# Optimization experiments

Hardware: AMD Instinct MI355X
Metric: run time of the kernel (lower is better)

Reference implementation:

```python
import jax, jax.numpy as jnp
import numpy as np

V = 6890          # SMPL vertex count
RAYS, POINTS = 256, 64
LATENT_DIM = 16
RES_HI, RES_LO = 10, 4


def posenc(x, res):
    # NeRF-style encoding: [x, sin(2^k x), cos(2^k x)] for k in 0..res-1 -> D*(1+2*res)
    freqs = 2.0 ** jnp.arange(res, dtype=x.dtype)            # [res]
    xf = x[..., None, :] * freqs[:, None]                    # [..., res, D]
    n = x.shape[:-1]
    s = jnp.sin(xf).reshape(*n, -1)
    c = jnp.cos(xf).reshape(*n, -1)
    return jnp.concatenate([x, s, c], axis=-1)


def setup_inputs() -> dict:
    key = jax.random.key(0)
    ks = jax.random.split(key, 12)
    inp = {}
    inp['pts'] = jax.random.normal(ks[0], (RAYS, POINTS, 6), jnp.float32)
    inp['keypoints'] = jax.random.normal(ks[1], (V, 3), jnp.float32)
    # invertible per-vertex 4x4 transforms: identity + small noise, stored [4,4,V]
    noise = 0.1 * jax.random.normal(ks[2], (4, 4, V), jnp.float32)
    inp['trans_kp'] = jnp.eye(4, dtype=jnp.float32)[:, :, None] + noise
    inp['neighbors'] = jax.random.randint(ks[3], (V, 7), 0, V, jnp.int32)
    inp['rest_pose'] = jax.random.normal(ks[4], (V, 3), jnp.float32)
    inp['latent'] = jax.random.normal(ks[5], (V, LATENT_DIM), jnp.float32)
    d_in = 7 * ((2 * RES_HI + 1) * 4 + LATENT_DIM)  # 700
    inp['W1'] = 0.05 * jax.random.normal(ks[6], (d_in, 256), jnp.float32)
    inp['b1'] = jnp.zeros((256,), jnp.float32)
    inp['W2'] = 0.05 * jax.random.normal(ks[7], (256, 256), jnp.float32)
    inp['b2'] = jnp.zeros((256,), jnp.float32)
    inp['W3'] = 0.05 * jax.random.normal(ks[8], (256, 256), jnp.float32)
    inp['b3'] = jnp.zeros((256,), jnp.float32)
    return inp


def reference(pts, keypoints, trans_kp, neighbors, rest_pose, latent,
              W1, b1, W2, b2, W3, b3):
    rays, points, _ = pts.shape
    p, view_dir = jnp.split(pts, 2, axis=-1)
    p = p.reshape(rays * points, 3)                          # [N,3]

    # brute-force 1-NN of p into keypoints
    d2 = ((p * p).sum(-1, keepdims=True)
          - 2.0 * p @ keypoints.T
          + (keypoints * keypoints).sum(-1))                 # [N,V]
    knn_index = jnp.argmin(d2, axis=1)                       # [N]

    # inverse transforms, keep rotation part: [3,3,V]
    T = jnp.linalg.inv(jnp.transpose(trans_kp, (2, 0, 1)))   # [V,4,4]
    R = jnp.transpose(T, (1, 2, 0))[:3, :3]                  # [3,3,V]

    vidx = neighbors[knn_index]                              # [N,7]
    vdist = p[:, None, :] - keypoints[vidx]                  # [N,7,3]

    diff = p - keypoints[knn_index]                          # [N,3]
    Rg = R[:, :, knn_index]                                  # [3,3,N]
    direction = jnp.einsum('ijn,nj->ni', Rg, diff)           # [N,3]
    nrm = jnp.linalg.norm(direction, axis=-1, keepdims=True)
    direction = direction / jnp.maximum(nrm, 1e-12)

    vfeat = jnp.concatenate(
        [rest_pose[vidx].reshape(-1, 21),
         jnp.linalg.norm(vdist, axis=-1)], axis=-1)          # [N,28]
    lfeat = latent[vidx].reshape(-1, 7 * latent.shape[1])    # [N,112]

    h = jnp.concatenate([posenc(vfeat, RES_HI), lfeat], -1)  # [N,700]
    h = jax.nn.relu(h @ W1 + b1)
    h = jax.nn.relu(h @ W2 + b2)
    h = h @ W3 + b3                                          # [N,256]

    out = jnp.concatenate([h, posenc(direction, RES_LO)], -1)  # [N,283]
    return out.reshape(rays, points, -1)
```

## Files before the change

kernel.cpp:

```cpp
#include <hip/hip_runtime.h>
#include <hip/hip_bf16.h>
#include <math.h>

#define V_N   6890
#define N_PTS 16384
#define D_IN  700
#define D_INP 704
#define D_HID 256
#define D_OUT 283
#define NCHUNK 32
#define CHUNK  216
#define GAP_EPS 1e-4f

#define RINV4_OFF 0
#define KP4_OFF   82688
#define RP4_OFF   110272
#define PB4_OFF   170640
#define WT1_OFF   2267792
#define WT2_OFF   2357904
#define WT3_OFF   2390672
#define X_OFF     2423440

typedef __attribute__((ext_vector_type(8))) short short8;
typedef __attribute__((ext_vector_type(4))) float f32x4;

__device__ __forceinline__ unsigned short f2bf(float f) {
    unsigned int u = __builtin_bit_cast(unsigned int, f);
    u += 0x7fffu + ((u >> 16) & 1u);
    return (unsigned short)(u >> 16);
}

__device__ __forceinline__ float fsin(float x) {
    return __builtin_amdgcn_sinf(__builtin_amdgcn_fractf(x * 0.15915494309189535f));
}
__device__ __forceinline__ float fcos(float x) {
    return __builtin_amdgcn_cosf(__builtin_amdgcn_fractf(x * 0.15915494309189535f));
}

__device__ __forceinline__ void glds16(const void* g, void* l) {
    __builtin_amdgcn_global_load_lds(
        (const __attribute__((address_space(1))) void*)g,
        (__attribute__((address_space(3))) void*)l, 16, 0, 0);
}

__device__ __forceinline__ int swzoff(int r, int sub) {
    return ((r << 2) | (sub ^ ((r >> 1) & 3))) << 4;
}

__device__ __forceinline__ int rescan64(const float* __restrict__ pts,
                                        const float4* __restrict__ kp4,
                                        int nn, int lane) {
    double pxd = (double)pts[nn*6+0], pyd = (double)pts[nn*6+1], pzd = (double)pts[nn*6+2];
    double ppd = pxd*pxd + pyd*pyd + pzd*pzd;
    double best = 1e300; int bbi = 0x7fffffff;
    for (int jj = lane; jj < V_N; jj += 64) {
        float4 k = kp4[jj];
        double kx = (double)k.x, ky = (double)k.y, kz = (double)k.z;
        double d = ppd - 2.0*(pxd*kx + pyd*ky + pzd*kz) + (kx*kx + ky*ky + kz*kz);
        if (d < best || (d == best && jj < bbi)) { best = d; bbi = jj; }
    }
#pragma unroll
    for (int off = 32; off >= 1; off >>= 1) {
        double od = __shfl_xor(best, off);
        int    oi = __shfl_xor(bbi, off);
        if (od < best || (od == best && oi < bbi)) { best = od; bbi = oi; }
    }
    return bbi;
}

#define SCAN_BLOCKS 2048
#define PREP_BLOCKS 27
__global__ __launch_bounds__(256) void prep_scan_kernel(
    const float* __restrict__ pts, const float* __restrict__ keyp,
    const float* __restrict__ trans, const float* __restrict__ restp,
    const float* __restrict__ W1, const float* __restrict__ W2,
    const float* __restrict__ W3,
    float4* __restrict__ rinv4, float4* __restrict__ kp4, float4* __restrict__ rp4,
    unsigned short* __restrict__ wt1, unsigned short* __restrict__ wt2,
    unsigned short* __restrict__ wt3, float4* __restrict__ pb4)
{
    __shared__ float4 s_kp[CHUNK];
    int bx = blockIdx.x, tid = threadIdx.x;

    if (bx < SCAN_BLOCKS) {
        int c = bx >> 6;
        int n = (bx & 63) * 256 + tid;
        int v0 = c * CHUNK;
        int nv = min(V_N - v0, CHUNK);
        if (tid < nv) {
            int v = v0 + tid;
            float kx = keyp[v*3+0], ky = keyp[v*3+1], kz = keyp[v*3+2];
            s_kp[tid] = make_float4(kx, ky, kz, kx*kx + ky*ky + kz*kz);
        }
        __syncthreads();

        float px2n = -2.0f * pts[n*6+0], py2n = -2.0f * pts[n*6+1], pz2n = -2.0f * pts[n*6+2];
        float m1 = 1e30f, m2 = 1e30f;
        int bi = 0x7fffffff;

#define KNN_STEP(kk, jj)                                                    \
    {                                                                       \
        float d = __builtin_fmaf(px2n, kk.x,                                \
                  __builtin_fmaf(py2n, kk.y,                                \
                  __builtin_fmaf(pz2n, kk.z, kk.w)));                       \
        bool lt = d < m1;                                                   \
        bi = lt ? (jj) : bi;                                                \
        m2 = __builtin_amdgcn_fmed3f(m1, m2, d);                            \
        m1 = fminf(m1, d);                                                  \
    }
        int j = 0;
        for (; j + 4 <= nv; j += 4) {
            float4 k0 = s_kp[j], k1 = s_kp[j+1], k2 = s_kp[j+2], k3 = s_kp[j+3];
            KNN_STEP(k0, v0+j); KNN_STEP(k1, v0+j+1);
            KNN_STEP(k2, v0+j+2); KNN_STEP(k3, v0+j+3);
        }
        for (; j < nv; ++j) {
            float4 k0 = s_kp[j];
            KNN_STEP(k0, v0+j);
        }
#undef KNN_STEP
        pb4[(size_t)n * NCHUNK + c] = make_float4(m1, m2, __int_as_float(bi), 0.0f);

    } else if (bx < SCAN_BLOCKS + PREP_BLOCKS) {
        int v = (bx - SCAN_BLOCKS) * 256 + tid;
        if (v >= V_N) return;
        float m[16];
#pragma unroll
        for (int i = 0; i < 16; ++i) m[i] = trans[i * V_N + v];

        float i0  =  m[5]*m[10]*m[15] - m[5]*m[11]*m[14] - m[9]*m[6]*m[15] + m[9]*m[7]*m[14] + m[13]*m[6]*m[11] - m[13]*m[7]*m[10];
        float i4  = -m[4]*m[10]*m[15] + m[4]*m[11]*m[14] + m[8]*m[6]*m[15] - m[8]*m[7]*m[14] - m[12]*m[6]*m[11] + m[12]*m[7]*m[10];
        float i8  =  m[4]*m[9]*m[15]  - m[4]*m[11]*m[13] - m[8]*m[5]*m[15] + m[8]*m[7]*m[13] + m[12]*m[5]*m[11] - m[12]*m[7]*m[9];
        float i12 = -m[4]*m[9]*m[14]  + m[4]*m[10]*m[13] + m[8]*m[5]*m[14] - m[8]*m[6]*m[13] - m[12]*m[5]*m[10] + m[12]*m[6]*m[9];
        float i1  = -m[1]*m[10]*m[15] + m[1]*m[11]*m[14] + m[9]*m[2]*m[15] - m[9]*m[3]*m[14] - m[13]*m[2]*m[11] + m[13]*m[3]*m[10];
        float i5  =  m[0]*m[10]*m[15] - m[0]*m[11]*m[14] - m[8]*m[2]*m[15] + m[8]*m[3]*m[14] + m[12]*m[2]*m[11] - m[12]*m[3]*m[10];
        float i9  = -m[0]*m[9]*m[15]  + m[0]*m[11]*m[13] + m[8]*m[1]*m[15] - m[8]*m[3]*m[13] - m[12]*m[1]*m[11] + m[12]*m[3]*m[9];
        float i2  =  m[1]*m[6]*m[15]  - m[1]*m[7]*m[14]  - m[5]*m[2]*m[15] + m[5]*m[3]*m[14] + m[13]*m[2]*m[7]  - m[13]*m[3]*m[6];
        float i6  = -m[0]*m[6]*m[15]  + m[0]*m[7]*m[14]  + m[4]*m[2]*m[15] - m[4]*m[3]*m[14] - m[12]*m[2]*m[7]  + m[12]*m[3]*m[6];
        float i10 =  m[0]*m[5]*m[15]  - m[0]*m[7]*m[13]  - m[4]*m[1]*m[15] + m[4]*m[3]*m[13] + m[12]*m[1]*m[7]  - m[12]*m[3]*m[5];

        float det = m[0]*i0 + m[1]*i4 + m[2]*i8 + m[3]*i12;
        float id = 1.0f / det;
        rinv4[v*3+0] = make_float4(i0*id, i1*id, i2*id, i4*id);
        rinv4[v*3+1] = make_float4(i5*id, i6*id, i8*id, i9*id);
        rinv4[v*3+2] = make_float4(i10*id, 0.0f, 0.0f, 0.0f);

        float kx = keyp[v*3], ky = keyp[v*3+1], kz = keyp[v*3+2];
        kp4[v] = make_float4(kx, ky, kz, kx*kx + ky*ky + kz*kz);
        rp4[v] = make_float4(restp[v*3], restp[v*3+1], restp[v*3+2], 0.0f);
    } else {
        int idx = (bx - SCAN_BLOCKS - PREP_BLOCKS) * 256 + tid;
        const int N1 = 256 * D_INP;
        const int N2 = 256 * 256;
        if (idx < N1) {
            int n = idx / D_INP, k = idx - n * D_INP;
            float v = (k < D_IN) ? W1[k * 256 + n] : 0.0f;
            wt1[n * D_INP + k] = f2bf(v);
        } else if (idx < N1 + N2) {
            int t = idx - N1;
            int n = t >> 8, k = t & 255;
            wt2[n * 256 + k] = f2bf(W2[k * 256 + n]);
        } else if (idx < N1 + 2 * N2) {
            int t = idx - N1 - N2;
            int n = t >> 8, k = t & 255;
            wt3[n * 256 + k] = f2bf(W3[k * 256 + n]);
        }
    }
}

__global__ __launch_bounds__(256) void feat_kernel(
    const float* __restrict__ pts, const int* __restrict__ neigh,
    const float* __restrict__ latent, const float4* __restrict__ rinv4,
    const float4* __restrict__ kp4, const float4* __restrict__ rp4,
    const float4* __restrict__ pb4, unsigned short* __restrict__ X,
    float* __restrict__ out)
{
    __shared__ float s_vf[4][2][29];
    __shared__ float s_dir[4][2][4];

    int t = threadIdx.x;
    int w = t >> 6, lane = t & 63;
    int n0 = blockIdx.x * 8 + w * 2;
    int ph = lane >> 5, g = lane & 31;

    float pxA = pts[n0*6+0],     pyA = pts[n0*6+1],     pzA = pts[n0*6+2];
    float pxB = pts[(n0+1)*6+0], pyB = pts[(n0+1)*6+1], pzB = pts[(n0+1)*6+2];

    float4 P = pb4[(size_t)(n0 + ph) * NCHUNK + g];
    float m1 = P.x, m2 = P.y;
    int   bi = __float_as_int(P.z);
#pragma unroll
    for (int off = 1; off <= 16; off <<= 1) {
        float o1 = __shfl_xor(m1, off);
        float o2 = __shfl_xor(m2, off);
        int   ob = __shfl_xor(bi, off);
        float nm2 = fminf(fminf(m2, o2), fmaxf(m1, o1));
        bool take = (o1 < m1) || (o1 == m1 && ob < bi);
        bi = take ? ob : bi;
        m1 = fminf(m1, o1);
        m2 = nm2;
    }
    unsigned long long ambmask = __ballot(m2 - m1 < GAP_EPS);
    if (ambmask & 1ull) {
        int r = rescan64(pts, kp4, n0, lane);
        if (ph == 0) bi = r;
    }
    if (ambmask & (1ull << 32)) {
        int r = rescan64(pts, kp4, n0 + 1, lane);
        if (ph == 1) bi = r;
    }

    int p = ph, j = g;
    int k8 = bi;
    float px = p ? pxB : pxA, py = p ? pyB : pyA, pz = p ? pzB : pzA;

    int v7 = 0;
    if (j < 7) {
        v7 = neigh[k8*7 + j];
        float4 kq = kp4[v7];
        float4 rq = rp4[v7];
        float dx = px - kq.x, dy = py - kq.y, dz = pz - kq.z;
        s_vf[w][p][j*3+0] = rq.x;
        s_vf[w][p][j*3+1] = rq.y;
        s_vf[w][p][j*3+2] = rq.z;
        s_vf[w][p][21+j]  = sqrtf(dx*dx + dy*dy + dz*dz);
    } else if (j == 7) {
        float4 kq = kp4[k8];
        float ddx = px - kq.x, ddy = py - kq.y, ddz = pz - kq.z;
        float4 R0 = rinv4[k8*3+0];
        float4 R1 = rinv4[k8*3+1];
        float4 R2 = rinv4[k8*3+2];
        float d0 = R0.x*ddx + R0.y*ddy + R0.z*ddz;
        float d1 = R0.w*ddx + R1.x*ddy + R1.y*ddz;
        float d2 = R1.z*ddx + R1.w*ddy + R2.x*ddz;
        float nrm = fmaxf(sqrtf(d0*d0 + d1*d1 + d2*d2), 1e-12f);
        s_dir[w][p][0] = d0/nrm; s_dir[w][p][1] = d1/nrm; s_dir[w][p][2] = d2/nrm;
    }

#pragma unroll
    for (int pp = 0; pp < 2; ++pp) {
        int n = n0 + pp;
        float dir0 = s_dir[w][pp][0];
        float dir1 = s_dir[w][pp][1];
        float dir2 = s_dir[w][pp][2];

        if (lane < 27) {
            float val;
            if (lane < 3) {
                val = (lane == 0) ? dir0 : (lane == 1) ? dir1 : dir2;
            } else {
                int tt = (lane < 15) ? lane - 3 : lane - 15;
                int m = tt % 3;
                float db = (m == 0) ? dir0 : (m == 1) ? dir1 : dir2;
                float a = db * (float)(1 << (tt/3));
                val = (lane < 15) ? fsin(a) : fcos(a);
            }
            out[(size_t)n*D_OUT + 256 + lane] = val;
        }

#pragma unroll
        for (int it = 0; it < 3; ++it) {
            int base = it * 256 + (lane << 2);
            bool in_range = base < D_INP;
            int region = (base < 28) ? 0 : (base < 308) ? 1 : (base < 588) ? 2
                       : (base < 700) ? 3 : 4;

            int t0 = (region == 1) ? base - 28 : (region == 2) ? base - 308 : 0;
            int q = t0 / 28;
            int r = t0 - q * 28;
            float f0 = (float)(1 << q);
            float a[4];
#pragma unroll
            for (int jj = 0; jj < 4; ++jj) {
                int rj; float fj;
                if (region == 0) { rj = base + jj; fj = 1.0f; }
                else if (region <= 2) {
                    rj = r + jj; fj = f0;
                    if (rj >= 28) { rj -= 28; fj = f0 * 2.0f; }
                } else { rj = 0; fj = 0.0f; }
                a[jj] = s_vf[w][pp][rj] * fj;
            }
            int idxc = (region == 3) ? (base - 588) >> 4 : 0;
            int vL = __shfl(v7, pp*32 + idxc);

            unsigned short r0, r1, r2, r3;
            if (region == 0) {
                r0 = f2bf(a[0]); r1 = f2bf(a[1]); r2 = f2bf(a[2]); r3 = f2bf(a[3]);
            } else if (region == 1) {
                r0 = f2bf(fsin(a[0])); r1 = f2bf(fsin(a[1]));
                r2 = f2bf(fsin(a[2])); r3 = f2bf(fsin(a[3]));
            } else if (region == 2) {
                r0 = f2bf(fcos(a[0])); r1 = f2bf(fcos(a[1]));
                r2 = f2bf(fcos(a[2])); r3 = f2bf(fcos(a[3]));
            } else if (region == 3) {
                int t3 = base - 588;
                float4 lv = *(const float4*)&latent[vL * 16 + (t3 & 15)];
                r0 = f2bf(lv.x); r1 = f2bf(lv.y); r2 = f2bf(lv.z); r3 = f2bf(lv.w);
            } else {
                r0 = r1 = r2 = r3 = 0;
            }
            if (in_range)
                *(ushort4*)&X[(size_t)n * D_INP + base] = make_ushort4(r0, r1, r2, r3);
        }
    }
}

#define HLD 264
__global__ __launch_bounds__(512) void mlp_kernel(
    const unsigned short* __restrict__ X,
    const unsigned short* __restrict__ wt1,
    const unsigned short* __restrict__ wt2,
    const unsigned short* __restrict__ wt3,
    const float* __restrict__ b1, const float* __restrict__ b2,
    const float* __restrict__ b3, float* __restrict__ out)
{
    __shared__ unsigned short As[64 * 32];
    __shared__ unsigned short Ws[256 * 32];
    __shared__ unsigned short H1[64 * HLD];
    __shared__ unsigned short H2[64 * HLD];

    int t = threadIdx.x, l = t & 63, w = t >> 6;
    int bm = blockIdx.x * 64;
    int mbase = (w >> 2) * 32, nbase = (w & 3) * 64;
    int lrow = l & 15, lk = (l >> 4) * 8, sub = l >> 4;
    int col0 = l & 15, rquad = (l >> 4) * 4;

    f32x4 acc[2][4];
    short8 af[2], bf[4];

#pragma unroll
    for (int mi = 0; mi < 2; ++mi)
#pragma unroll
        for (int ni = 0; ni < 4; ++ni) acc[mi][ni] = {0.f, 0.f, 0.f, 0.f};

    for (int k0 = 0; k0 < D_INP; k0 += 32) {
        if (t < 256) {
            int r = t >> 2;
            int sg = (t & 3) ^ ((r >> 1) & 3);
            glds16(X + (size_t)(bm + r) * D_INP + k0 + sg * 8, (char*)As + t * 16);
        }
#pragma unroll
        for (int i = 0; i < 2; ++i) {
            int c = i * 512 + t;
            int r = c >> 2;
            int sg = (c & 3) ^ ((r >> 1) & 3);
            glds16(wt1 + (size_t)r * D_INP + k0 + sg * 8, (char*)Ws + (size_t)c * 16);
        }
        __syncthreads();
#pragma unroll
        for (int mi = 0; mi < 2; ++mi)
            af[mi] = *(const short8*)((const char*)As + swzoff(mbase + mi*16 + lrow, sub));
#pragma unroll
        for (int ni = 0; ni < 4; ++ni)
            bf[ni] = *(const short8*)((const char*)Ws + swzoff(nbase + ni*16 + lrow, sub));
#pragma unroll
        for (int mi = 0; mi < 2; ++mi)
#pragma unroll
            for (int ni = 0; ni < 4; ++ni)
                acc[mi][ni] = __builtin_amdgcn_mfma_f32_16x16x32_bf16(
                    af[mi], bf[ni], acc[mi][ni], 0, 0, 0);
        __syncthreads();
    }
#pragma unroll
    for (int mi = 0; mi < 2; ++mi)
#pragma unroll
        for (int ni = 0; ni < 4; ++ni) {
            int col = nbase + ni * 16 + col0;
            float bv = b1[col];
#pragma unroll
            for (int r = 0; r < 4; ++r) {
                int row = mbase + mi * 16 + rquad + r;
                H1[row * HLD + col] = f2bf(fmaxf(acc[mi][ni][r] + bv, 0.0f));
            }
        }
    __syncthreads();

#pragma unroll
    for (int mi = 0; mi < 2; ++mi)
#pragma unroll
        for (int ni = 0; ni < 4; ++ni) acc[mi][ni] = {0.f, 0.f, 0.f, 0.f};

    for (int k0 = 0; k0 < D_HID; k0 += 32) {
#pragma unroll
        for (int i = 0; i < 2; ++i) {
            int c = i * 512 + t;
            int r = c >> 2;
            int sg = (c & 3) ^ ((r >> 1) & 3);
            glds16(wt2 + (size_t)r * D_HID + k0 + sg * 8, (char*)Ws + (size_t)c * 16);
        }
        __syncthreads();
#pragma unroll
        for (int mi = 0; mi < 2; ++mi)
            af[mi] = *(const short8*)&H1[(mbase + mi * 16 + lrow) * HLD + k0 + lk];
#pragma unroll
        for (int ni = 0; ni < 4; ++ni)
            bf[ni] = *(const short8*)((const char*)Ws + swzoff(nbase + ni*16 + lrow, sub));
#pragma unroll
        for (int mi = 0; mi < 2; ++mi)
#pragma unroll
            for (int ni = 0; ni < 4; ++ni)
                acc[mi][ni] = __builtin_amdgcn_mfma_f32_16x16x32_bf16(
                    af[mi], bf[ni], acc[mi][ni], 0, 0, 0);
        __syncthreads();
    }
#pragma unroll
    for (int mi = 0; mi < 2; ++mi)
#pragma unroll
        for (int ni = 0; ni < 4; ++ni) {
            int col = nbase + ni * 16 + col0;
            float bv = b2[col];
#pragma unroll
            for (int r = 0; r < 4; ++r) {
                int row = mbase + mi * 16 + rquad + r;
                H2[row * HLD + col] = f2bf(fmaxf(acc[mi][ni][r] + bv, 0.0f));
            }
        }
    __syncthreads();

#pragma unroll
    for (int mi = 0; mi < 2; ++mi)
#pragma unroll
        for (int ni = 0; ni < 4; ++ni) acc[mi][ni] = {0.f, 0.f, 0.f, 0.f};

    for (int k0 = 0; k0 < D_HID; k0 += 32) {
#pragma unroll
        for (int i = 0; i < 2; ++i) {
            int c = i * 512 + t;
            int r = c >> 2;
            int sg = (c & 3) ^ ((r >> 1) & 3);
            glds16(wt3 + (size_t)r * D_HID + k0 + sg * 8, (char*)Ws + (size_t)c * 16);
        }
        __syncthreads();
#pragma unroll
        for (int mi = 0; mi < 2; ++mi)
            af[mi] = *(const short8*)&H2[(mbase + mi * 16 + lrow) * HLD + k0 + lk];
#pragma unroll
        for (int ni = 0; ni < 4; ++ni)
            bf[ni] = *(const short8*)((const char*)Ws + swzoff(nbase + ni*16 + lrow, sub));
#pragma unroll
        for (int mi = 0; mi < 2; ++mi)
#pragma unroll
            for (int ni = 0; ni < 4; ++ni)
                acc[mi][ni] = __builtin_amdgcn_mfma_f32_16x16x32_bf16(
                    af[mi], bf[ni], acc[mi][ni], 0, 0, 0);
        __syncthreads();
    }
#pragma unroll
    for (int mi = 0; mi < 2; ++mi)
#pragma unroll
        for (int ni = 0; ni < 4; ++ni) {
            int col = nbase + ni * 16 + col0;
            float bv = b3[col];
#pragma unroll
            for (int r = 0; r < 4; ++r) {
                int row = bm + mbase + mi * 16 + rquad + r;
                out[(size_t)row * D_OUT + col] = acc[mi][ni][r] + bv;
            }
        }
}

extern "C" void kernel_launch(void* const* d_in, const int* in_sizes, int n_in,
                              void* d_out, int out_size, void* d_ws, size_t ws_size,
                              hipStream_t stream) {
    const float* pts    = (const float*)d_in[0];
    const float* keyp   = (const float*)d_in[1];
    const float* trans  = (const float*)d_in[2];
    const int*   neigh  = (const int*)d_in[3];
    const float* restp  = (const float*)d_in[4];
    const float* latent = (const float*)d_in[5];
    const float* W1     = (const float*)d_in[6];
    const float* b1     = (const float*)d_in[7];
    const float* W2     = (const float*)d_in[8];
    const float* b2     = (const float*)d_in[9];
    const float* W3     = (const float*)d_in[10];
    const float* b3     = (const float*)d_in[11];
    float* out = (float*)d_out;

    float* wsf = (float*)d_ws;
    float4*         rinv4 = (float4*)(wsf + RINV4_OFF);
    float4*         kp4   = (float4*)(wsf + KP4_OFF);
    float4*         rp4   = (float4*)(wsf + RP4_OFF);
    float4*         pb4   = (float4*)(wsf + PB4_OFF);
    unsigned short* wt1   = (unsigned short*)(wsf + WT1_OFF);
    unsigned short* wt2   = (unsigned short*)(wsf + WT2_OFF);
    unsigned short* wt3   = (unsigned short*)(wsf + WT3_OFF);
    unsigned short* X     = (unsigned short*)(wsf + X_OFF);

    int wconv_blocks = (256*D_INP + 2*256*256 + 255) / 256;
    prep_scan_kernel<<<SCAN_BLOCKS + PREP_BLOCKS + wconv_blocks, 256, 0, stream>>>(
        pts, keyp, trans, restp, W1, W2, W3, rinv4, kp4, rp4, wt1, wt2, wt3, pb4);
    feat_kernel<<<N_PTS/8, 256, 0, stream>>>(pts, neigh, latent, rinv4,
                                             kp4, rp4, pb4, X, out);
    mlp_kernel<<<N_PTS/64, 512, 0, stream>>>(X, wt1, wt2, wt3, b1, b2, b3, out);
}
```

Before: 173.7 us.

## Double-buffer MLP shared-memory tiles and widen KNN unroll to eight

The MLP kernel now keeps two shared-memory buffers for the activation and weight tiles and issues the next K-slice's global-to-LDS loads before computing on the current one. It also prefetches the first weight tile of layers 2 and 3 during the previous layer's epilogue. The point is to hide global load latency behind the MFMA work and to drop one barrier per K step. Separately, the KNN scan inner loop is unrolled by 8 instead of 4. This raises LDS use, which may lower occupancy, and raises register pressure in the scan.

```diff
diff --git a/kernel.cpp b/kernel.cpp
--- a/kernel.cpp
+++ b/kernel.cpp
@@ -109,10 +109,13 @@
         m1 = fminf(m1, d);                                                  \
     }
         int j = 0;
-        for (; j + 4 <= nv; j += 4) {
-            float4 k0 = s_kp[j], k1 = s_kp[j+1], k2 = s_kp[j+2], k3 = s_kp[j+3];
-            KNN_STEP(k0, v0+j); KNN_STEP(k1, v0+j+1);
+        for (; j + 8 <= nv; j += 8) {
+            float4 k0 = s_kp[j],   k1 = s_kp[j+1], k2 = s_kp[j+2], k3 = s_kp[j+3];
+            float4 k4 = s_kp[j+4], k5 = s_kp[j+5], k6 = s_kp[j+6], k7 = s_kp[j+7];
+            KNN_STEP(k0, v0+j);   KNN_STEP(k1, v0+j+1);
             KNN_STEP(k2, v0+j+2); KNN_STEP(k3, v0+j+3);
+            KNN_STEP(k4, v0+j+4); KNN_STEP(k5, v0+j+5);
+            KNN_STEP(k6, v0+j+6); KNN_STEP(k7, v0+j+7);
         }
         for (; j < nv; ++j) {
             float4 k0 = s_kp[j];
@@ -314,8 +317,8 @@
     const float* __restrict__ b1, const float* __restrict__ b2,
     const float* __restrict__ b3, float* __restrict__ out)
 {
-    __shared__ unsigned short As[64 * 32];
-    __shared__ unsigned short Ws[256 * 32];
+    __shared__ unsigned short As[2][64 * 32];
+    __shared__ unsigned short Ws[2][256 * 32];
     __shared__ unsigned short H1[64 * HLD];
     __shared__ unsigned short H2[64 * HLD];
 
@@ -328,31 +331,44 @@
     f32x4 acc[2][4];
     short8 af[2], bf[4];
 
-#pragma unroll
-    for (int mi = 0; mi < 2; ++mi)
-#pragma unroll
-        for (int ni = 0; ni < 4; ++ni) acc[mi][ni] = {0.f, 0.f, 0.f, 0.f};
-
-    for (int k0 = 0; k0 < D_INP; k0 += 32) {
+    auto stageA = [&](int buf, int k0) {
         if (t < 256) {
-            int r = t >> 2;
-            int sg = (t & 3) ^ ((r >> 1) & 3);
-            glds16(X + (size_t)(bm + r) * D_INP + k0 + sg * 8, (char*)As + t * 16);
-        }
+            int r = t >> 2, sg = (t & 3) ^ ((r >> 1) & 3);
+            glds16(X + (size_t)(bm + r) * D_INP + k0 + sg * 8,
+                   (char*)As[buf] + t * 16);
+        }
+    };
+    auto stageW = [&](int buf, const unsigned short* wsrc, int ld, int k0) {
 #pragma unroll
         for (int i = 0; i < 2; ++i) {
             int c = i * 512 + t;
-            int r = c >> 2;
-            int sg = (c & 3) ^ ((r >> 1) & 3);
-            glds16(wt1 + (size_t)r * D_INP + k0 + sg * 8, (char*)Ws + (size_t)c * 16);
-        }
-        __syncthreads();
+            int r = c >> 2, sg = (c & 3) ^ ((r >> 1) & 3);
+            glds16(wsrc + (size_t)r * ld + k0 + sg * 8,
+                   (char*)Ws[buf] + (size_t)c * 16);
+        }
+    };
+
+#pragma unroll
+    for (int mi = 0; mi < 2; ++mi)
+#pragma unroll
+        for (int ni = 0; ni < 4; ++ni) acc[mi][ni] = {0.f, 0.f, 0.f, 0.f};
+
+    stageA(0, 0);
+    stageW(0, wt1, D_INP, 0);
+    __syncthreads();
+    const int NK1 = D_INP / 32;
+    for (int ks = 0; ks < NK1; ++ks) {
+        int cur = ks & 1;
+        if (ks + 1 < NK1) {
+            stageA(cur ^ 1, (ks + 1) * 32);
+            stageW(cur ^ 1, wt1, D_INP, (ks + 1) * 32);
+        }
 #pragma unroll
         for (int mi = 0; mi < 2; ++mi)
-            af[mi] = *(const short8*)((const char*)As + swzoff(mbase + mi*16 + lrow, sub));
+            af[mi] = *(const short8*)((const char*)As[cur] + swzoff(mbase + mi*16 + lrow, sub));
 #pragma unroll
         for (int ni = 0; ni < 4; ++ni)
-            bf[ni] = *(const short8*)((const char*)Ws + swzoff(nbase + ni*16 + lrow, sub));
+            bf[ni] = *(const short8*)((const char*)Ws[cur] + swzoff(nbase + ni*16 + lrow, sub));
 #pragma unroll
         for (int mi = 0; mi < 2; ++mi)
 #pragma unroll
@@ -361,6 +377,7 @@
                     af[mi], bf[ni], acc[mi][ni], 0, 0, 0);
         __syncthreads();
     }
+    stageW(0, wt2, D_HID, 0);
 #pragma unroll
     for (int mi = 0; mi < 2; ++mi)
 #pragma unroll
@@ -380,21 +397,16 @@
 #pragma unroll
         for (int ni = 0; ni < 4; ++ni) acc[mi][ni] = {0.f, 0.f, 0.f, 0.f};
 
-    for (int k0 = 0; k0 < D_HID; k0 += 32) {
-#pragma unroll
-        for (int i = 0; i < 2; ++i) {
-            int c = i * 512 + t;
-            int r = c >> 2;
-            int sg = (c & 3) ^ ((r >> 1) & 3);
-            glds16(wt2 + (size_t)r * D_HID + k0 + sg * 8, (char*)Ws + (size_t)c * 16);
-        }
-        __syncthreads();
+    const int NK2 = D_HID / 32;
+    for (int ks = 0; ks < NK2; ++ks) {
+        int cur = ks & 1;
+        if (ks + 1 < NK2) stageW(cur ^ 1, wt2, D_HID, (ks + 1) * 32);
 #pragma unroll
         for (int mi = 0; mi < 2; ++mi)
-            af[mi] = *(const short8*)&H1[(mbase + mi * 16 + lrow) * HLD + k0 + lk];
+            af[mi] = *(const short8*)&H1[(mbase + mi * 16 + lrow) * HLD + ks * 32 + lk];
 #pragma unroll
         for (int ni = 0; ni < 4; ++ni)
-            bf[ni] = *(const short8*)((const char*)Ws + swzoff(nbase + ni*16 + lrow, sub));
+            bf[ni] = *(const short8*)((const char*)Ws[cur] + swzoff(nbase + ni*16 + lrow, sub));
 #pragma unroll
         for (int mi = 0; mi < 2; ++mi)
 #pragma unroll
@@ -403,6 +415,7 @@
                     af[mi], bf[ni], acc[mi][ni], 0, 0, 0);
         __syncthreads();
     }
+    stageW(0, wt3, D_HID, 0);
 #pragma unroll
     for (int mi = 0; mi < 2; ++mi)
 #pragma unroll
@@ -422,21 +435,15 @@
 #pragma unroll
         for (int ni = 0; ni < 4; ++ni) acc[mi][ni] = {0.f, 0.f, 0.f, 0.f};
 
-    for (int k0 = 0; k0 < D_HID; k0 += 32) {
-#pragma unroll
-        for (int i = 0; i < 2; ++i) {
-            int c = i * 512 + t;
-            int r = c >> 2;
-            int sg = (c & 3) ^ ((r >> 1) & 3);
-            glds16(wt3 + (size_t)r * D_HID + k0 + sg * 8, (char*)Ws + (size_t)c * 16);
-        }
-        __syncthreads();
+    for (int ks = 0; ks < NK2; ++ks) {
+        int cur = ks & 1;
+        if (ks + 1 < NK2) stageW(cur ^ 1, wt3, D_HID, (ks + 1) * 32);
 #pragma unroll
         for (int mi = 0; mi < 2; ++mi)
-            af[mi] = *(const short8*)&H2[(mbase + mi * 16 + lrow) * HLD + k0 + lk];
+            af[mi] = *(const short8*)&H2[(mbase + mi * 16 + lrow) * HLD + ks * 32 + lk];
 #pragma unroll
         for (int ni = 0; ni < 4; ++ni)
-            bf[ni] = *(const short8*)((const char*)Ws + swzoff(nbase + ni*16 + lrow, sub));
+            bf[ni] = *(const short8*)((const char*)Ws[cur] + swzoff(nbase + ni*16 + lrow, sub));
 #pragma unroll
         for (int mi = 0; mi < 2; ++mi)
 #pragma unroll
```

Result: no change. 173.9 us (+0.1%).
